# Kernel optimization log

Measured on AMD Instinct MI355X. Metric: run time of the kernel, lower is better.

## Reference

```python
import jax, jax.numpy as jnp
from jax import lax
import numpy as np
import math

EMBED_DIM = 1024
NUM_HEADS = 16
REDUCTION = 2


def setup_inputs() -> dict:
    key = jax.random.key(0)
    ks = jax.random.split(key, 11)
    B, N, C = 2, 4096, EMBED_DIM
    s = 1.0 / math.sqrt(C)
    return {
        "x": jax.random.normal(ks[0], (B, N, C), jnp.float32),
        "q_w": jax.random.normal(ks[1], (C, C), jnp.float32) * s,
        "q_b": jax.random.normal(ks[2], (C,), jnp.float32) * s,
        "k_w": jax.random.normal(ks[3], (C, C), jnp.float32) * s,
        "k_b": jax.random.normal(ks[4], (C,), jnp.float32) * s,
        "v_w": jax.random.normal(ks[5], (C, C), jnp.float32) * s,
        "v_b": jax.random.normal(ks[6], (C,), jnp.float32) * s,
        "conv_w": jax.random.normal(ks[7], (C, 1, 3), jnp.float32) * 0.5,
        "conv_b": jax.random.normal(ks[8], (C,), jnp.float32) * 0.1,
        "out_w": jax.random.normal(ks[9], (C, C), jnp.float32) * s,
        "out_b": jax.random.normal(ks[10], (C,), jnp.float32) * s,
    }


def reference(x, q_w, q_b, k_w, k_b, v_w, v_b, conv_w, conv_b, out_w, out_b):
    B, N, C = x.shape
    H = NUM_HEADS
    D = C // H
    scale = 1.0 / math.sqrt(D)

    q = x @ q_w.T + q_b  # [B,N,C]

    # depthwise conv1d KV downsample: kernel=3, stride=REDUCTION, pad=1, groups=C
    xd = jnp.transpose(x, (0, 2, 1))  # [B,C,N]
    xd = lax.conv_general_dilated(
        xd, conv_w, window_strides=(REDUCTION,), padding=[(1, 1)],
        feature_group_count=C, dimension_numbers=("NCH", "OIH", "NCH"))
    xd = xd + conv_b[None, :, None]
    xd = jnp.transpose(xd, (0, 2, 1))  # [B,Nk,C]

    k = xd @ k_w.T + k_b
    v = xd @ v_w.T + v_b

    Nk = k.shape[1]
    q = q.reshape(B, N, H, D).transpose(0, 2, 1, 3)   # [B,H,N,D]
    k = k.reshape(B, Nk, H, D).transpose(0, 2, 1, 3)  # [B,H,Nk,D]
    v = v.reshape(B, Nk, H, D).transpose(0, 2, 1, 3)

    att = jnp.einsum("bhnd,bhmd->bhnm", q, k) * scale  # [B,H,N,Nk]
    att = jax.nn.softmax(att, axis=-1)
    out = jnp.einsum("bhnm,bhmd->bhnd", att, v)        # [B,H,N,D]
    out = out.transpose(0, 2, 1, 3).reshape(B, N, C)
    return out @ out_w.T + out_b
```

## Files before the change

kernel.cpp:

```cpp
#include <hip/hip_runtime.h>
#include <stdint.h>
#include <stddef.h>


using bf16x8 = __attribute__((ext_vector_type(8))) short;
using f32x4  = __attribute__((ext_vector_type(4))) float;
using f32x16 = __attribute__((ext_vector_type(16))) float;
using u16x4  = __attribute__((ext_vector_type(4))) unsigned short;
using u32x4  = __attribute__((ext_vector_type(4))) uint32_t;

#if defined(__has_builtin)
#if __has_builtin(__builtin_amdgcn_exp2f)
#define FAST_EXP2(x) __builtin_amdgcn_exp2f(x)
#endif
#endif
#ifndef FAST_EXP2
extern "C" __device__ float __ocml_native_exp2_f32(float);
#define FAST_EXP2(x) __ocml_native_exp2_f32(x)
#endif

__device__ __forceinline__ unsigned short f2bf(float f) {
  union { float f; uint32_t u; } v; v.f = f;
  uint32_t r = v.u + 0x7fffu + ((v.u >> 16) & 1u);
  return (unsigned short)(r >> 16);
}

__device__ __forceinline__ uint32_t cvt_pk_bf16(float lo, float hi) {
  uint32_t r;
  asm("v_cvt_pk_bf16_f32 %0, %1, %2" : "=v"(r) : "v"(lo), "v"(hi));
  return r;
}

__device__ __forceinline__ void plane32_swap(uint32_t& a, uint32_t& b) {
  asm("v_permlane32_swap_b32 %0, %1" : "+v"(a), "+v"(b));
}

__global__ __launch_bounds__(256)
void cast_bf16_kernel(const float* __restrict__ in, unsigned short* __restrict__ out, int n) {
  int i = (blockIdx.x * 256 + threadIdx.x) * 8;
  if (i >= n) return;
  float4 a = *(const float4*)(in + i);
  float4 b = *(const float4*)(in + i + 4);
  u16x4 r0 = {f2bf(a.x), f2bf(a.y), f2bf(a.z), f2bf(a.w)};
  u16x4 r1 = {f2bf(b.x), f2bf(b.y), f2bf(b.z), f2bf(b.w)};
  *(u16x4*)(out + i) = r0;
  *(u16x4*)(out + i + 4) = r1;
}

struct WPtrs { const float* p0; const float* p1; const float* p2; const float* p3; };
__global__ __launch_bounds__(256)
void cast4_bf16_kernel(WPtrs in, unsigned short* __restrict__ out) {
  int which = blockIdx.x >> 9;
  int i = ((blockIdx.x & 511) * 256 + threadIdx.x) * 8;
  const float* src = (which == 0) ? in.p0 : (which == 1) ? in.p1
                   : (which == 2) ? in.p2 : in.p3;
  unsigned short* dst = out + (size_t)which * 1048576;
  float4 a = *(const float4*)(src + i);
  float4 b = *(const float4*)(src + i + 4);
  u16x4 r0 = {f2bf(a.x), f2bf(a.y), f2bf(a.z), f2bf(a.w)};
  u16x4 r1 = {f2bf(b.x), f2bf(b.y), f2bf(b.z), f2bf(b.w)};
  *(u16x4*)(dst + i) = r0;
  *(u16x4*)(dst + i + 4) = r1;
}

__global__ __launch_bounds__(256)
void conv_ds_kernel(const float* __restrict__ x, const float* __restrict__ cw,
                    const float* __restrict__ cb, unsigned short* __restrict__ xd) {
  int row = blockIdx.x;
  int b = row >> 11, m = row & 2047;
  int c = threadIdx.x * 4;
  const float* xb = x + (size_t)b * 4096 * 1024;
  int n0 = 2 * m - 1;
  float4 x0 = {0.f, 0.f, 0.f, 0.f};
  if (n0 >= 0) x0 = *(const float4*)(xb + (size_t)n0 * 1024 + c);
  float4 x1 = *(const float4*)(xb + (size_t)(2 * m) * 1024 + c);
  float4 x2 = *(const float4*)(xb + (size_t)(2 * m + 1) * 1024 + c);
  float4 w0 = *(const float4*)(cw + c * 3);
  float4 w1 = *(const float4*)(cw + c * 3 + 4);
  float4 w2 = *(const float4*)(cw + c * 3 + 8);
  float4 bb = *(const float4*)(cb + c);
  float r0 = x0.x * w0.x + x1.x * w0.y + x2.x * w0.z + bb.x;
  float r1 = x0.y * w0.w + x1.y * w1.x + x2.y * w1.y + bb.y;
  float r2 = x0.z * w1.z + x1.z * w1.w + x2.z * w2.x + bb.z;
  float r3 = x0.w * w2.y + x1.w * w2.z + x2.w * w2.w + bb.w;
  u16x4 r = {f2bf(r0), f2bf(r1), f2bf(r2), f2bf(r3)};
  *(u16x4*)(xd + (size_t)row * 1024 + c) = r;
}

template<int OUT_MODE>
__global__ __launch_bounds__(256)
void gemm_bt(const unsigned short* __restrict__ A, const unsigned short* __restrict__ W,
             const float* __restrict__ bias, const float* __restrict__ bias2,
             void* __restrict__ out, void* __restrict__ out2,
             int M, int N, int K) {
  __shared__ unsigned short As[128 * 32];
  __shared__ unsigned short Bs[128 * 32];
  const int tid = threadIdx.x;
  const int w = tid >> 6, lane = tid & 63;
  const int nbn = N >> 7;
  const int bm = blockIdx.x / nbn, bn = blockIdx.x % nbn;
  const int wr = w >> 1, wc = w & 1;
  const int l15 = lane & 15, l4 = lane >> 4;

  f32x4 acc[4][4];
#pragma unroll
  for (int m = 0; m < 4; ++m)
#pragma unroll
    for (int n = 0; n < 4; ++n) acc[m][n] = (f32x4)0.0f;

  const int arow = bm * 128 + w * 16 + (lane >> 2);
  const int brow = bn * 128 + w * 16 + (lane >> 2);
  const int kcol = (lane & 3) * 8;

  for (int kt = 0; kt < K; kt += 32) {
#pragma unroll
    for (int p = 0; p < 2; ++p) {
      __builtin_amdgcn_global_load_lds(
          (const __attribute__((address_space(1))) void*)(A + (size_t)(arow + p * 64) * K + kt + kcol),
          (__attribute__((address_space(3))) void*)(As + p * 2048 + w * 512), 16, 0, 0);
      __builtin_amdgcn_global_load_lds(
          (const __attribute__((address_space(1))) void*)(W + (size_t)(brow + p * 64) * K + kt + kcol),
          (__attribute__((address_space(3))) void*)(Bs + p * 2048 + w * 512), 16, 0, 0);
    }
    __syncthreads();
    bf16x8 af[4], bf[4];
#pragma unroll
    for (int m = 0; m < 4; ++m) af[m] = *(const bf16x8*)(As + (wr * 64 + m * 16 + l15) * 32 + l4 * 8);
#pragma unroll
    for (int n = 0; n < 4; ++n) bf[n] = *(const bf16x8*)(Bs + (wc * 64 + n * 16 + l15) * 32 + l4 * 8);
#pragma unroll
    for (int m = 0; m < 4; ++m)
#pragma unroll
      for (int n = 0; n < 4; ++n)
        acc[m][n] = __builtin_amdgcn_mfma_f32_16x16x32_bf16(af[m], bf[n], acc[m][n], 0, 0, 0);
    __syncthreads();
  }

  const bool vregion = (OUT_MODE == 3) && (bn >= 8);
#pragma unroll
  for (int n = 0; n < 4; ++n) {
    int col = bn * 128 + wc * 64 + n * 16 + l15;
    float bv = vregion ? bias2[col - 1024] : bias[col];
#pragma unroll
    for (int m = 0; m < 4; ++m) {
      int row0 = bm * 128 + wr * 64 + m * 16 + l4 * 4;
      if (vregion) {
        int b = row0 >> 11, kv = row0 & 2047;
        u16x4 r = {f2bf(acc[m][n][0] + bv), f2bf(acc[m][n][1] + bv),
                   f2bf(acc[m][n][2] + bv), f2bf(acc[m][n][3] + bv)};
        *(u16x4*)((unsigned short*)out2 + ((size_t)(b * 1024 + (col - 1024))) * 2048 + kv) = r;
      } else if (OUT_MODE == 1 || OUT_MODE == 3) {
        const int ldn = (OUT_MODE == 3) ? 1024 : N;
#pragma unroll
        for (int i = 0; i < 4; ++i)
          ((unsigned short*)out)[(size_t)(row0 + i) * ldn + col] = f2bf(acc[m][n][i] + bv);
      } else {
#pragma unroll
        for (int i = 0; i < 4; ++i)
          ((float*)out)[(size_t)(row0 + i) * N + col] = acc[m][n][i] + bv;
      }
    }
  }
}

#define ATT_SCL_L2E 0.18033688011112043f

__global__ __launch_bounds__(256)
void flash_attn_kernel(const unsigned short* __restrict__ q,
                       const unsigned short* __restrict__ k,
                       const unsigned short* __restrict__ vt,
                       unsigned short* __restrict__ o) {
  const int bid = blockIdx.x;
  const int lin = (bid & 7) * 128 + (bid >> 3);
  const int qb = lin & 31;
  const int hb = lin >> 5;
  const int h = hb & 15, b = hb >> 4;

  const int tid = threadIdx.x;
  const int w = tid >> 6, lane = tid & 63;
  const int l31 = lane & 31, hi = lane >> 5;

  __shared__ unsigned short Ks[2][64 * 64];
  __shared__ unsigned short Vs[2][64 * 64];

  const size_t C = 1024;
  const int qrow = b * 4096 + qb * 128 + w * 32 + l31;

  bf16x8 qf[4];
#pragma unroll
  for (int ks = 0; ks < 4; ++ks)
    qf[ks] = *(const bf16x8*)(q + (size_t)qrow * C + h * 64 + ks * 16 + hi * 8);

  f32x16 o0 = (f32x16)0.0f, o1 = (f32x16)0.0f;
  float lrun = 0.f;

  const int srow = (tid & 7) | ((tid >> 5) << 3);
  const int sc2  = (tid >> 3) & 3;
  const int sxor = (srow & 7);
  const unsigned short* kbase = k  + ((size_t)(b * 2048 + srow)) * C + h * 64;
  const unsigned short* vbase = vt + ((size_t)(b * 1024 + h * 64 + srow)) * 2048;

  bf16x8 krg[2], vrg[2];
#pragma unroll
  for (int j = 0; j < 2; ++j) {
    krg[j] = *(const bf16x8*)(kbase + (sc2 + 4 * j) * 8);
    vrg[j] = *(const bf16x8*)(vbase + (sc2 + 4 * j) * 8);
  }
#pragma unroll
  for (int j = 0; j < 2; ++j) {
    int ph = ((sc2 + 4 * j) ^ sxor) * 8;
    *(bf16x8*)(&Ks[0][srow * 64 + ph]) = krg[j];
    *(bf16x8*)(&Vs[0][srow * 64 + ph]) = vrg[j];
  }
#pragma unroll
  for (int j = 0; j < 2; ++j) {
    krg[j] = *(const bf16x8*)(kbase + (size_t)64 * C + (sc2 + 4 * j) * 8);
    vrg[j] = *(const bf16x8*)(vbase + 64 + (sc2 + 4 * j) * 8);
  }
  __syncthreads();

  const int r0 = l31, r1 = 32 + l31;
  const int x0c = (r0 & 7) * 8, x1c = (r1 & 7) * 8;

  for (int t = 0; t < 32; ++t) {
    const unsigned short* Kc = Ks[t & 1];
    const unsigned short* Vc = Vs[t & 1];
    unsigned short* Kn = (unsigned short*)Ks[(t & 1) ^ 1];
    unsigned short* Vn = (unsigned short*)Vs[(t & 1) ^ 1];

    f32x16 s0 = (f32x16)0.0f, s1 = (f32x16)0.0f;
    __builtin_amdgcn_s_setprio(1);
#pragma unroll
    for (int ks = 0; ks < 4; ++ks) {
      int coff = ks * 16 + hi * 8;
      bf16x8 kf0 = *(const bf16x8*)(Kc + r0 * 64 + (coff ^ x0c));
      bf16x8 kf1 = *(const bf16x8*)(Kc + r1 * 64 + (coff ^ x1c));
      s0 = __builtin_amdgcn_mfma_f32_32x32x16_bf16(kf0, qf[ks], s0, 0, 0, 0);
      s1 = __builtin_amdgcn_mfma_f32_32x32x16_bf16(kf1, qf[ks], s1, 0, 0, 0);
    }
    __builtin_amdgcn_s_setprio(0);

    if (t < 31) {
#pragma unroll
      for (int j = 0; j < 2; ++j) {
        int ph = ((sc2 + 4 * j) ^ sxor) * 8;
        *(bf16x8*)(Kn + srow * 64 + ph) = krg[j];
        *(bf16x8*)(Vn + srow * 64 + ph) = vrg[j];
      }
    }
    if (t < 30) {
#pragma unroll
      for (int j = 0; j < 2; ++j) {
        krg[j] = *(const bf16x8*)(kbase + (size_t)(t + 2) * 64 * C + (sc2 + 4 * j) * 8);
        vrg[j] = *(const bf16x8*)(vbase + (t + 2) * 64 + (sc2 + 4 * j) * 8);
      }
    }

    float rs0 = 0.f, rs1 = 0.f;
#pragma unroll
    for (int i = 0; i < 16; ++i) {
      float p0 = FAST_EXP2(s0[i] * ATT_SCL_L2E);
      float p1 = FAST_EXP2(s1[i] * ATT_SCL_L2E);
      s0[i] = p0; s1[i] = p1;
      rs0 += p0; rs1 += p1;
    }
    lrun += rs0 + rs1;

    u32x4 pw[4];
#pragma unroll
    for (int hh = 0; hh < 2; ++hh) {
#pragma unroll
      for (int cp = 0; cp < 2; ++cp) {
#pragma unroll
        for (int e = 0; e < 2; ++e) {
          float xa0 = (hh == 0) ? s0[8 * cp + 2 * e]     : s1[8 * cp + 2 * e];
          float xa1 = (hh == 0) ? s0[8 * cp + 2 * e + 1] : s1[8 * cp + 2 * e + 1];
          float xb0 = (hh == 0) ? s0[8 * cp + 4 + 2 * e]     : s1[8 * cp + 4 + 2 * e];
          float xb1 = (hh == 0) ? s0[8 * cp + 4 + 2 * e + 1] : s1[8 * cp + 4 + 2 * e + 1];
          uint32_t wa = cvt_pk_bf16(xa0, xa1);
          uint32_t wb = cvt_pk_bf16(xb0, xb1);
          plane32_swap(wa, wb);
          pw[2 * hh + cp][e]     = wa;
          pw[2 * hh + cp][e + 2] = wb;
        }
      }
    }

    __builtin_amdgcn_s_setprio(1);
#pragma unroll
    for (int ksv = 0; ksv < 4; ++ksv) {
      bf16x8 pv = __builtin_bit_cast(bf16x8, pw[ksv]);
      int coff = ksv * 16 + hi * 8;
      bf16x8 vf0 = *(const bf16x8*)(Vc + r0 * 64 + (coff ^ x0c));
      bf16x8 vf1 = *(const bf16x8*)(Vc + r1 * 64 + (coff ^ x1c));
      o0 = __builtin_amdgcn_mfma_f32_32x32x16_bf16(vf0, pv, o0, 0, 0, 0);
      o1 = __builtin_amdgcn_mfma_f32_32x32x16_bf16(vf1, pv, o1, 0, 0, 0);
    }
    __builtin_amdgcn_s_setprio(0);

    if (t < 31) __syncthreads();
  }

  float lsum = lrun + __shfl_xor(lrun, 32);
  const float inv = 1.0f / lsum;
  u32x4 ow[4];
#pragma unroll
  for (int c = 0; c < 4; ++c) {
#pragma unroll
    for (int e = 0; e < 2; ++e) {
      uint32_t wa = cvt_pk_bf16(o0[4 * c + 2 * e] * inv, o0[4 * c + 2 * e + 1] * inv);
      uint32_t wb = cvt_pk_bf16(o1[4 * c + 2 * e] * inv, o1[4 * c + 2 * e + 1] * inv);
      plane32_swap(wa, wb);
      ow[c][e]     = wa;
      ow[c][e + 2] = wb;
    }
  }
  unsigned short* op = o + (size_t)qrow * C + h * 64 + hi * 32;
#pragma unroll
  for (int ch = 0; ch < 4; ++ch)
    *(u32x4*)(op + ch * 8) = ow[ch];
}

extern "C" void kernel_launch(void* const* d_in, const int* in_sizes, int n_in,
                              void* d_out, int out_size, void* d_ws, size_t ws_size,
                              hipStream_t stream) {
  const float* x   = (const float*)d_in[0];
  const float* q_w = (const float*)d_in[1];
  const float* q_b = (const float*)d_in[2];
  const float* k_w = (const float*)d_in[3];
  const float* k_b = (const float*)d_in[4];
  const float* v_w = (const float*)d_in[5];
  const float* v_b = (const float*)d_in[6];
  const float* cw  = (const float*)d_in[7];
  const float* cb  = (const float*)d_in[8];
  const float* o_w = (const float*)d_in[9];
  const float* o_b = (const float*)d_in[10];
  float* out = (float*)d_out;

  unsigned short* ws    = (unsigned short*)d_ws;
  unsigned short* x_bf  = ws;
  unsigned short* qw_bf = x_bf + 8388608;
  unsigned short* kw_bf = qw_bf + 1048576;
  unsigned short* vw_bf = kw_bf + 1048576;
  unsigned short* ow_bf = vw_bf + 1048576;
  unsigned short* q_bf  = ow_bf + 1048576;
  unsigned short* xd_bf = q_bf + 8388608;
  unsigned short* k_bf  = xd_bf + 4194304;
  unsigned short* vt_bf = k_bf + 4194304;
  unsigned short* ao_bf = x_bf;

  cast_bf16_kernel<<<4096, 256, 0, stream>>>(x, x_bf, 8388608);
  WPtrs wp = {q_w, k_w, v_w, o_w};
  cast4_bf16_kernel<<<2048, 256, 0, stream>>>(wp, qw_bf);
  conv_ds_kernel<<<4096, 256, 0, stream>>>(x, cw, cb, xd_bf);

  gemm_bt<1><<<512, 256, 0, stream>>>(x_bf, qw_bf, q_b, nullptr, q_bf, nullptr,
                                      8192, 1024, 1024);
  gemm_bt<3><<<512, 256, 0, stream>>>(xd_bf, kw_bf, k_b, v_b, k_bf, vt_bf,
                                      4096, 2048, 1024);

  flash_attn_kernel<<<1024, 256, 0, stream>>>(q_bf, k_bf, vt_bf, ao_bf);

  gemm_bt<0><<<512, 256, 0, stream>>>(ao_bf, ow_bf, o_b, nullptr, out, nullptr,
                                      8192, 1024, 1024);
}
```

Baseline: 218.8 us.

## Software-pipeline QK^T for the next tile against softmax and PV of the current

Restructures the attention loop so the QK^T MFMAs for tile t+1 are issued alongside the exp/convert and PV MFMAs of tile t, ping-ponging two sets of score accumulators. K is now staged two tiles ahead in shared memory while V stays one tile ahead, and the prologue fills both K buffers. The goal is to keep the matrix units busy while the exponential and conversion work runs. In exchange it needs 32 more accumulator registers, which may lower occupancy. The prologue also contains a redundant, discarded MFMA pass.

Result: faster. 209.7 us (-4.1%).

```diff
diff --git a/kernel.cpp b/kernel.cpp
--- a/kernel.cpp
+++ b/kernel.cpp
@@ -200,21 +200,25 @@
   const unsigned short* kbase = k  + ((size_t)(b * 2048 + srow)) * C + h * 64;
   const unsigned short* vbase = vt + ((size_t)(b * 1024 + h * 64 + srow)) * 2048;
 
-  bf16x8 krg[2], vrg[2];
+  bf16x8 krg[2], vrg[2], tmp[2];
+#pragma unroll
+  for (int j = 0; j < 2; ++j) tmp[j] = *(const bf16x8*)(kbase + (sc2 + 4 * j) * 8);
+#pragma unroll
+  for (int j = 0; j < 2; ++j)
+    *(bf16x8*)(&Ks[0][srow * 64 + (((sc2 + 4 * j) ^ sxor) * 8)]) = tmp[j];
+#pragma unroll
+  for (int j = 0; j < 2; ++j) tmp[j] = *(const bf16x8*)(kbase + (size_t)64 * C + (sc2 + 4 * j) * 8);
+#pragma unroll
+  for (int j = 0; j < 2; ++j)
+    *(bf16x8*)(&Ks[1][srow * 64 + (((sc2 + 4 * j) ^ sxor) * 8)]) = tmp[j];
+#pragma unroll
+  for (int j = 0; j < 2; ++j) tmp[j] = *(const bf16x8*)(vbase + (sc2 + 4 * j) * 8);
+#pragma unroll
+  for (int j = 0; j < 2; ++j)
+    *(bf16x8*)(&Vs[0][srow * 64 + (((sc2 + 4 * j) ^ sxor) * 8)]) = tmp[j];
 #pragma unroll
   for (int j = 0; j < 2; ++j) {
-    krg[j] = *(const bf16x8*)(kbase + (sc2 + 4 * j) * 8);
-    vrg[j] = *(const bf16x8*)(vbase + (sc2 + 4 * j) * 8);
-  }
-#pragma unroll
-  for (int j = 0; j < 2; ++j) {
-    int ph = ((sc2 + 4 * j) ^ sxor) * 8;
-    *(bf16x8*)(&Ks[0][srow * 64 + ph]) = krg[j];
-    *(bf16x8*)(&Vs[0][srow * 64 + ph]) = vrg[j];
-  }
-#pragma unroll
-  for (int j = 0; j < 2; ++j) {
-    krg[j] = *(const bf16x8*)(kbase + (size_t)64 * C + (sc2 + 4 * j) * 8);
+    krg[j] = *(const bf16x8*)(kbase + (size_t)128 * C + (sc2 + 4 * j) * 8);
     vrg[j] = *(const bf16x8*)(vbase + 64 + (sc2 + 4 * j) * 8);
   }
   __syncthreads();
@@ -222,46 +226,57 @@
   const int r0 = l31, r1 = 32 + l31;
   const int x0c = (r0 & 7) * 8, x1c = (r1 & 7) * 8;
 
-  for (int t = 0; t < 32; ++t) {
-    const unsigned short* Kc = Ks[t & 1];
+  f32x16 sA0 = (f32x16)0.0f, sA1 = (f32x16)0.0f;
+  f32x16 sB0 = (f32x16)0.0f, sB1 = (f32x16)0.0f;
+  __builtin_amdgcn_s_setprio(1);
+#pragma unroll
+  for (int ks = 0; ks < 4; ++ks) {
+    int coff = ks * 16 + hi * 8;
+    bf16x8 kf0 = *(const bf16x8*)(&Ks[0][r0 * 64 + (coff ^ x0c)]);
+    bf16x8 kf1 = *(const bf16x8*)(&Ks[0][r1 * 64 + (coff ^ x1c)]);
+    sA0 = __builtin_amdgcn_mfma_f32_32x32x16_bf16(kf0, qf[0 + ks - ks], sA0, 0, 0, 0);
+    sA0 = sA0;
+    sA0 = __builtin_amdgcn_mfma_f32_32x32x16_bf16(kf0, qf[ks], sA0, 0, 0, 0);
+    sA1 = __builtin_amdgcn_mfma_f32_32x32x16_bf16(kf1, qf[ks], sA1, 0, 0, 0);
+  }
+  __builtin_amdgcn_s_setprio(0);
+  sA0 = (f32x16)0.0f; sA1 = (f32x16)0.0f;
+  __builtin_amdgcn_s_setprio(1);
+#pragma unroll
+  for (int ks = 0; ks < 4; ++ks) {
+    int coff = ks * 16 + hi * 8;
+    bf16x8 kf0 = *(const bf16x8*)(&Ks[0][r0 * 64 + (coff ^ x0c)]);
+    bf16x8 kf1 = *(const bf16x8*)(&Ks[0][r1 * 64 + (coff ^ x1c)]);
+    sA0 = __builtin_amdgcn_mfma_f32_32x32x16_bf16(kf0, qf[ks], sA0, 0, 0, 0);
+    sA1 = __builtin_amdgcn_mfma_f32_32x32x16_bf16(kf1, qf[ks], sA1, 0, 0, 0);
+  }
+  __builtin_amdgcn_s_setprio(0);
+  __syncthreads();
+
+  auto body = [&](int t, f32x16& c0, f32x16& c1, f32x16& n0, f32x16& n1) {
     const unsigned short* Vc = Vs[t & 1];
-    unsigned short* Kn = (unsigned short*)Ks[(t & 1) ^ 1];
-    unsigned short* Vn = (unsigned short*)Vs[(t & 1) ^ 1];
-
-    f32x16 s0 = (f32x16)0.0f, s1 = (f32x16)0.0f;
-    __builtin_amdgcn_s_setprio(1);
-#pragma unroll
-    for (int ks = 0; ks < 4; ++ks) {
-      int coff = ks * 16 + hi * 8;
-      bf16x8 kf0 = *(const bf16x8*)(Kc + r0 * 64 + (coff ^ x0c));
-      bf16x8 kf1 = *(const bf16x8*)(Kc + r1 * 64 + (coff ^ x1c));
-      s0 = __builtin_amdgcn_mfma_f32_32x32x16_bf16(kf0, qf[ks], s0, 0, 0, 0);
-      s1 = __builtin_amdgcn_mfma_f32_32x32x16_bf16(kf1, qf[ks], s1, 0, 0, 0);
-    }
-    __builtin_amdgcn_s_setprio(0);
 
     if (t < 31) {
-#pragma unroll
-      for (int j = 0; j < 2; ++j) {
-        int ph = ((sc2 + 4 * j) ^ sxor) * 8;
-        *(bf16x8*)(Kn + srow * 64 + ph) = krg[j];
-        *(bf16x8*)(Vn + srow * 64 + ph) = vrg[j];
+      const unsigned short* Kn = Ks[(t + 1) & 1];
+      n0 = (f32x16)0.0f; n1 = (f32x16)0.0f;
+      __builtin_amdgcn_s_setprio(1);
+#pragma unroll
+      for (int ks = 0; ks < 4; ++ks) {
+        int coff = ks * 16 + hi * 8;
+        bf16x8 kf0 = *(const bf16x8*)(Kn + r0 * 64 + (coff ^ x0c));
+        bf16x8 kf1 = *(const bf16x8*)(Kn + r1 * 64 + (coff ^ x1c));
+        n0 = __builtin_amdgcn_mfma_f32_32x32x16_bf16(kf0, qf[ks], n0, 0, 0, 0);
+        n1 = __builtin_amdgcn_mfma_f32_32x32x16_bf16(kf1, qf[ks], n1, 0, 0, 0);
       }
-    }
-    if (t < 30) {
-#pragma unroll
-      for (int j = 0; j < 2; ++j) {
-        krg[j] = *(const bf16x8*)(kbase + (size_t)(t + 2) * 64 * C + (sc2 + 4 * j) * 8);
-        vrg[j] = *(const bf16x8*)(vbase + (t + 2) * 64 + (sc2 + 4 * j) * 8);
-      }
+      __builtin_amdgcn_s_setprio(0);
     }
 
     float rs0 = 0.f, rs1 = 0.f;
 #pragma unroll
     for (int i = 0; i < 16; ++i) {
-      float p0 = FAST_EXP2(s0[i] * ATT_SCL_L2E);
-      float p1 = FAST_EXP2(s1[i] * ATT_SCL_L2E);
-      s0[i] = p0; s1[i] = p1;
+      float p0 = FAST_EXP2(c0[i] * ATT_SCL_L2E);
+      float p1 = FAST_EXP2(c1[i] * ATT_SCL_L2E);
+      c0[i] = p0; c1[i] = p1;
       rs0 += p0; rs1 += p1;
     }
     lrun += rs0 + rs1;
@@ -273,10 +288,10 @@
       for (int cp = 0; cp < 2; ++cp) {
 #pragma unroll
         for (int e = 0; e < 2; ++e) {
-          float xa0 = (hh == 0) ? s0[8 * cp + 2 * e]     : s1[8 * cp + 2 * e];
-          float xa1 = (hh == 0) ? s0[8 * cp + 2 * e + 1] : s1[8 * cp + 2 * e + 1];
-          float xb0 = (hh == 0) ? s0[8 * cp + 4 + 2 * e]     : s1[8 * cp + 4 + 2 * e];
-          float xb1 = (hh == 0) ? s0[8 * cp + 4 + 2 * e + 1] : s1[8 * cp + 4 + 2 * e + 1];
+          float xa0 = (hh == 0) ? c0[8 * cp + 2 * e]     : c1[8 * cp + 2 * e];
+          float xa1 = (hh == 0) ? c0[8 * cp + 2 * e + 1] : c1[8 * cp + 2 * e + 1];
+          float xb0 = (hh == 0) ? c0[8 * cp + 4 + 2 * e]     : c1[8 * cp + 4 + 2 * e];
+          float xb1 = (hh == 0) ? c0[8 * cp + 4 + 2 * e + 1] : c1[8 * cp + 4 + 2 * e + 1];
           uint32_t wa = cvt_pk_bf16(xa0, xa1);
           uint32_t wb = cvt_pk_bf16(xb0, xb1);
           plane32_swap(wa, wb);
@@ -298,7 +313,32 @@
     }
     __builtin_amdgcn_s_setprio(0);
 
+    if (t < 30) {
+#pragma unroll
+      for (int j = 0; j < 2; ++j)
+        *(bf16x8*)(&((unsigned short*)Ks[t & 1])[srow * 64 + (((sc2 + 4 * j) ^ sxor) * 8)]) = krg[j];
+    }
+    if (t < 31) {
+#pragma unroll
+      for (int j = 0; j < 2; ++j)
+        *(bf16x8*)(&((unsigned short*)Vs[(t + 1) & 1])[srow * 64 + (((sc2 + 4 * j) ^ sxor) * 8)]) = vrg[j];
+    }
+    if (t < 29) {
+#pragma unroll
+      for (int j = 0; j < 2; ++j)
+        krg[j] = *(const bf16x8*)(kbase + (size_t)(t + 3) * 64 * C + (sc2 + 4 * j) * 8);
+    }
+    if (t < 30) {
+#pragma unroll
+      for (int j = 0; j < 2; ++j)
+        vrg[j] = *(const bf16x8*)(vbase + (t + 2) * 64 + (sc2 + 4 * j) * 8);
+    }
     if (t < 31) __syncthreads();
+  };
+
+  for (int tt = 0; tt < 16; ++tt) {
+    body(2 * tt,     sA0, sA1, sB0, sB1);
+    body(2 * tt + 1, sB0, sB1, sA0, sA1);
   }
 
   float lsum = lrun + __shfl_xor(lrun, 32);
```
